# Kernel optimization log

Hardware: AMD Instinct MI355X
Metric: run time of the kernel (lower is better)

The kernel has to match this reference:

```python
import jax, jax.numpy as jnp
import numpy as np
import math

B, WIN, C_IN, C_OUT = 8, 512, 38, 38
D_MODEL, N_HEADS, E_LAYERS, D_FF = 512, 8, 3, 512
EH = D_MODEL // N_HEADS
LN_EPS = 1e-3  # keras LayerNormalization default


def setup_inputs() -> dict:
    key = jax.random.key(0)
    ks = jax.random.split(key, 24)
    s = 0.02
    rn = lambda k, sh: jax.random.normal(k, sh, jnp.float32) * s
    L, d, H = E_LAYERS, D_MODEL, N_HEADS
    return {
        "x": jax.random.normal(ks[0], (B, WIN, C_IN), jnp.float32),
        "conv_k": rn(ks[1], (3, C_IN, d)),
        "Wq": rn(ks[2], (L, d, d)), "bq": jnp.zeros((L, d), jnp.float32),
        "Wk": rn(ks[3], (L, d, d)), "bk": jnp.zeros((L, d), jnp.float32),
        "Wv": rn(ks[4], (L, d, d)), "bv": jnp.zeros((L, d), jnp.float32),
        "Ws": rn(ks[5], (L, d, H)), "bs": jnp.zeros((L, H), jnp.float32),
        "Wo": rn(ks[6], (L, d, d)), "bo": jnp.zeros((L, d), jnp.float32),
        "W1": rn(ks[7], (L, d, D_FF)), "b1": jnp.zeros((L, D_FF), jnp.float32),
        "W2": rn(ks[8], (L, D_FF, d)), "b2": jnp.zeros((L, d), jnp.float32),
        "ln1_g": jnp.ones((L, d), jnp.float32), "ln1_b": jnp.zeros((L, d), jnp.float32),
        "ln2_g": jnp.ones((L, d), jnp.float32), "ln2_b": jnp.zeros((L, d), jnp.float32),
        "lnf_g": jnp.ones((d,), jnp.float32), "lnf_b": jnp.zeros((d,), jnp.float32),
        "Wp": rn(ks[9], (d, C_OUT)), "bp": jnp.zeros((C_OUT,), jnp.float32),
    }


def _layernorm(x, g, b):
    mu = jnp.mean(x, axis=-1, keepdims=True)
    var = jnp.mean((x - mu) ** 2, axis=-1, keepdims=True)
    return (x - mu) * jax.lax.rsqrt(var + LN_EPS) * g + b


def _pos_embedding():
    pos = jnp.arange(WIN, dtype=jnp.float32)[:, None]
    div = jnp.exp(jnp.arange(0, D_MODEL, 2, dtype=jnp.float32) * (-math.log(10000.0) / D_MODEL))
    # interleave sin at even idx, cos at odd idx
    return jnp.stack([jnp.sin(pos * div), jnp.cos(pos * div)], axis=-1).reshape(WIN, D_MODEL)


def reference(x, conv_k, Wq, bq, Wk, bk, Wv, bv, Ws, bs, Wo, bo,
              W1, b1, W2, b2, ln1_g, ln1_b, ln2_g, ln2_b, lnf_g, lnf_b, Wp, bp):
    # --- DataEmbedding: wrap-pad then Conv1D(k=3, valid), plus sinusoidal PE ---
    xp = jnp.concatenate([x[:, -1:], x, x[:, :1]], axis=1)
    h = jax.lax.conv_general_dilated(xp, conv_k, window_strides=(1,), padding='VALID',
                                     dimension_numbers=('NWC', 'WIO', 'NWC'))
    h = h + _pos_embedding()[None]

    idx = jnp.arange(WIN, dtype=jnp.float32)
    dist = jnp.abs(idx[:, None] - idx[None, :])
    scale = 1.0 / math.sqrt(EH)
    inv_sqrt_2pi = 1.0 / math.sqrt(2.0 * math.pi)

    series_l, prior_l, sigma_l = [], [], []
    for i in range(E_LAYERS):
        q = (h @ Wq[i] + bq[i]).reshape(B, WIN, N_HEADS, EH)
        k = (h @ Wk[i] + bk[i]).reshape(B, WIN, N_HEADS, EH)
        v = (h @ Wv[i] + bv[i]).reshape(B, WIN, N_HEADS, EH)
        sig = h @ Ws[i] + bs[i]

        scores = jnp.einsum('blhe,bshe->bhls', q, k)  # mask_flag=False in model
        series = jax.nn.softmax(scores * scale, axis=-1)  # [B, H, L, S]

        sg = jnp.transpose(sig, (0, 2, 1))               # [B, H, L]
        sg = jax.nn.sigmoid(sg * 5.0) + 1e-5
        sg = jnp.power(3.0, sg) - 1.0
        sg4 = jnp.broadcast_to(sg[..., None], (B, N_HEADS, WIN, WIN))
        prior = inv_sqrt_2pi / sg4 * jnp.exp(-(dist ** 2) / (2.0 * sg4 ** 2))

        attn_out = jnp.einsum('bhls,bshd->blhd', series, v).reshape(B, WIN, D_MODEL)
        h = _layernorm(h + attn_out @ Wo[i] + bo[i], ln1_g[i], ln1_b[i])
        y = jax.nn.gelu(h @ W1[i] + b1[i], approximate=False)
        y = y @ W2[i] + b2[i]
        h = _layernorm(h + y, ln2_g[i], ln2_b[i])

        series_l.append(series); prior_l.append(prior); sigma_l.append(sg4)

    h = _layernorm(h, lnf_g, lnf_b)
    out = h @ Wp + bp
    return (out, jnp.stack(series_l), jnp.stack(prior_l), jnp.stack(sigma_l))
```

## Files before the change

### kernel.cpp

```cpp
#include <hip/hip_runtime.h>
#include <math.h>


typedef unsigned short ushort;
typedef __attribute__((ext_vector_type(8))) ushort ushort8;
typedef __attribute__((ext_vector_type(8))) short short8;
typedef __attribute__((ext_vector_type(4))) float float4v;

__device__ inline ushort f2bf(float f) {
  union { float f; unsigned u; } v; v.f = f;
  return (ushort)((v.u + 0x7fffu + ((v.u >> 16) & 1u)) >> 16);
}

__global__ __launch_bounds__(512) void embed_kernel(const float* __restrict__ x,
                                                    const float* __restrict__ ck,
                                                    float* __restrict__ h) {
  int bt = blockIdx.x;
  int b = bt >> 9, t = bt & 511;
  int co = threadIdx.x;
  __shared__ float xs[3][38];
  if (co < 114) {
    int w = co / 38, ci = co - w * 38;
    int r = (t - 1 + w + 512) & 511;
    xs[w][ci] = x[((long)(b << 9) + r) * 38 + ci];
  }
  __syncthreads();
  float acc = 0.f;
#pragma unroll
  for (int w = 0; w < 3; ++w)
#pragma unroll
    for (int ci = 0; ci < 38; ++ci)
      acc = fmaf(xs[w][ci], ck[(w * 38 + ci) * 512 + co], acc);
  float div = expf((float)(co & ~1) * (-9.210340371976184f / 512.f));
  float ang = (float)t * div;
  float pe = (co & 1) ? cosf(ang) : sinf(ang);
  h[(long)bt * 512 + co] = acc + pe;
}

__global__ __launch_bounds__(256) void wcvt_kernel(const float* __restrict__ W,
                                                   ushort* __restrict__ Wt,
                                                   long lstride) {
  int l = blockIdx.z;
  int n = blockIdx.x * 256 + threadIdx.x;
  int k0 = blockIdx.y * 8;
  const float* w = W + (long)l * 262144;
  ushort* o = Wt + (long)l * lstride;
  ushort8 v;
#pragma unroll
  for (int i = 0; i < 8; ++i) v[i] = f2bf(w[(long)(k0 + i) * 512 + n]);
  *(ushort8*)&o[(long)n * 512 + k0] = v;
}

__global__ __launch_bounds__(512) void bcat_kernel(const float* __restrict__ bq,
                                                   const float* __restrict__ bk,
                                                   const float* __restrict__ bv,
                                                   float* __restrict__ bqkv) {
  int l = blockIdx.x, t = threadIdx.x;
  bqkv[l * 1536 + t] = bq[l * 512 + t];
  bqkv[l * 1536 + 512 + t] = bk[l * 512 + t];
  bqkv[l * 1536 + 1024 + t] = bv[l * 512 + t];
}

template <bool ABF16, bool GELU_, bool CBF16>
__global__ __launch_bounds__(256) void gemm_mfma(
    const void* __restrict__ Av, int lda,
    const ushort* __restrict__ B, int ldb,
    const float* __restrict__ bias,
    void* __restrict__ Cv, int ldc,
    int K, float alpha) {
  __shared__ ushort As[64 * 40];
  __shared__ ushort Bs[64 * 40];
  int t = threadIdx.x;
  int m0 = blockIdx.y * 64, n0 = blockIdx.x * 64;
  int w = t >> 6, lane = t & 63;
  int wr = (w >> 1) * 32, wc = (w & 1) * 32;
  int fm = lane & 15, koff = (lane >> 4) * 8;

  float4v acc[2][2] = {{{0.f, 0.f, 0.f, 0.f}, {0.f, 0.f, 0.f, 0.f}},
                       {{0.f, 0.f, 0.f, 0.f}, {0.f, 0.f, 0.f, 0.f}}};
  int sm = t >> 2, skq = (t & 3) * 8;

  for (int k0 = 0; k0 < K; k0 += 32) {
    if (ABF16) {
      const ushort* Ab = (const ushort*)Av;
      *(ushort8*)&As[sm * 40 + skq] =
          *(const ushort8*)&Ab[(long)(m0 + sm) * lda + k0 + skq];
    } else {
      const float* Af = (const float*)Av;
      const float* ap = &Af[(long)(m0 + sm) * lda + k0 + skq];
      float4 x0 = *(const float4*)ap;
      float4 x1 = *(const float4*)(ap + 4);
      ushort8 v;
      v[0] = f2bf(x0.x); v[1] = f2bf(x0.y); v[2] = f2bf(x0.z); v[3] = f2bf(x0.w);
      v[4] = f2bf(x1.x); v[5] = f2bf(x1.y); v[6] = f2bf(x1.z); v[7] = f2bf(x1.w);
      *(ushort8*)&As[sm * 40 + skq] = v;
    }
    *(ushort8*)&Bs[sm * 40 + skq] =
        *(const ushort8*)&B[(long)(n0 + sm) * ldb + k0 + skq];
    __syncthreads();

    short8 a0 = *(const short8*)&As[(wr + fm) * 40 + koff];
    short8 a1 = *(const short8*)&As[(wr + 16 + fm) * 40 + koff];
    short8 b0 = *(const short8*)&Bs[(wc + fm) * 40 + koff];
    short8 b1 = *(const short8*)&Bs[(wc + 16 + fm) * 40 + koff];
    acc[0][0] = __builtin_amdgcn_mfma_f32_16x16x32_bf16(a0, b0, acc[0][0], 0, 0, 0);
    acc[0][1] = __builtin_amdgcn_mfma_f32_16x16x32_bf16(a0, b1, acc[0][1], 0, 0, 0);
    acc[1][0] = __builtin_amdgcn_mfma_f32_16x16x32_bf16(a1, b0, acc[1][0], 0, 0, 0);
    acc[1][1] = __builtin_amdgcn_mfma_f32_16x16x32_bf16(a1, b1, acc[1][1], 0, 0, 0);
    __syncthreads();
  }

#pragma unroll
  for (int j = 0; j < 2; ++j) {
    int col = n0 + wc + 16 * j + fm;
    float bv = bias ? bias[col] : 0.f;
#pragma unroll
    for (int i = 0; i < 2; ++i) {
#pragma unroll
      for (int r = 0; r < 4; ++r) {
        int row = m0 + wr + 16 * i + (lane >> 4) * 4 + r;
        float v = acc[i][j][r] * alpha + bv;
        if (GELU_) v = 0.5f * v * (1.f + erff(v * 0.7071067811865476f));
        if (CBF16)
          ((ushort*)Cv)[(long)row * ldc + col] = f2bf(v);
        else
          ((float*)Cv)[(long)row * ldc + col] = v;
      }
    }
  }
}

__global__ __launch_bounds__(256, 1) void attn_fused(
    const ushort* __restrict__ qkv, const float* __restrict__ sg,
    float* __restrict__ series, float* __restrict__ prior,
    float* __restrict__ sigma, float* __restrict__ t1) {
  __shared__ ushort KPs[36864];
  __shared__ ushort Qs[4608];
  __shared__ ushort Vc[4608];
  __shared__ float red[256];

  int t = threadIdx.x;
  int m0 = blockIdx.x * 64;
  int bh = blockIdx.y;
  int b = bh >> 3, hh = bh & 7;
  int w = t >> 6, lane = t & 63;
  int fm = lane & 15, q4 = lane >> 4;
  int wc = w * 128;
  long rowg = (long)b * 512;

  {
    int row = t >> 2, kq = (t & 3) * 16;
    const ushort* src = &qkv[(rowg + m0 + row) * 1536 + hh * 64 + kq];
    *(ushort8*)&Qs[row * 72 + kq] = *(const ushort8*)src;
    *(ushort8*)&Qs[row * 72 + kq + 8] = *(const ushort8*)(src + 8);
#pragma unroll
    for (int p = 0; p < 8; ++p) {
      int srow = p * 64 + row;
      const ushort* ks = &qkv[(rowg + srow) * 1536 + 512 + hh * 64 + kq];
      *(ushort8*)&KPs[srow * 72 + kq] = *(const ushort8*)ks;
      *(ushort8*)&KPs[srow * 72 + kq + 8] = *(const ushort8*)(ks + 8);
    }
  }
  __syncthreads();

  float4v acc[4][8];
#pragma unroll
  for (int i = 0; i < 4; ++i)
#pragma unroll
    for (int j = 0; j < 8; ++j) acc[i][j] = (float4v){0.f, 0.f, 0.f, 0.f};

#pragma unroll
  for (int ks = 0; ks < 2; ++ks) {
    int ko = ks * 32 + q4 * 8;
    short8 a[4], bfr[8];
#pragma unroll
    for (int i = 0; i < 4; ++i)
      a[i] = *(const short8*)&Qs[(16 * i + fm) * 72 + ko];
#pragma unroll
    for (int j = 0; j < 8; ++j)
      bfr[j] = *(const short8*)&KPs[(wc + 16 * j + fm) * 72 + ko];
#pragma unroll
    for (int i = 0; i < 4; ++i)
#pragma unroll
      for (int j = 0; j < 8; ++j)
        acc[i][j] = __builtin_amdgcn_mfma_f32_16x16x32_bf16(a[i], bfr[j], acc[i][j], 0, 0, 0);
  }

#pragma unroll
  for (int i = 0; i < 4; ++i)
#pragma unroll
    for (int j = 0; j < 8; ++j)
#pragma unroll
      for (int r = 0; r < 4; ++r) acc[i][j][r] *= 0.125f;

  float mrow[4][4];
#pragma unroll
  for (int i = 0; i < 4; ++i)
#pragma unroll
    for (int r = 0; r < 4; ++r) {
      float m = acc[i][0][r];
#pragma unroll
      for (int j = 1; j < 8; ++j) m = fmaxf(m, acc[i][j][r]);
#pragma unroll
      for (int off = 1; off < 16; off <<= 1) m = fmaxf(m, __shfl_xor(m, off));
      mrow[i][r] = m;
    }
  if (fm == 0) {
#pragma unroll
    for (int i = 0; i < 4; ++i)
#pragma unroll
      for (int r = 0; r < 4; ++r)
        red[(16 * i + q4 * 4 + r) * 4 + w] = mrow[i][r];
  }
  __syncthreads();
#pragma unroll
  for (int i = 0; i < 4; ++i)
#pragma unroll
    for (int r = 0; r < 4; ++r) {
      const float* rp = &red[(16 * i + q4 * 4 + r) * 4];
      mrow[i][r] = fmaxf(fmaxf(rp[0], rp[1]), fmaxf(rp[2], rp[3]));
    }
  float lrow[4][4];
#pragma unroll
  for (int i = 0; i < 4; ++i)
#pragma unroll
    for (int r = 0; r < 4; ++r) {
      float s = 0.f;
#pragma unroll
      for (int j = 0; j < 8; ++j) {
        float e = __expf(acc[i][j][r] - mrow[i][r]);
        acc[i][j][r] = e;
        s += e;
      }
#pragma unroll
      for (int off = 1; off < 16; off <<= 1) s += __shfl_xor(s, off);
      lrow[i][r] = s;
    }
  __syncthreads();
  if (fm == 0) {
#pragma unroll
    for (int i = 0; i < 4; ++i)
#pragma unroll
      for (int r = 0; r < 4; ++r)
        red[(16 * i + q4 * 4 + r) * 4 + w] = lrow[i][r];
  }
  __syncthreads();
#pragma unroll
  for (int i = 0; i < 4; ++i)
#pragma unroll
    for (int r = 0; r < 4; ++r) {
      const float* rp = &red[(16 * i + q4 * 4 + r) * 4];
      lrow[i][r] = 1.f / (rp[0] + rp[1] + rp[2] + rp[3]);
    }

  float* serp = series + ((long)bh << 18);
#pragma unroll
  for (int i = 0; i < 4; ++i)
#pragma unroll
    for (int r = 0; r < 4; ++r) {
      int row = 16 * i + q4 * 4 + r;
      float inv = lrow[i][r];
#pragma unroll
      for (int j = 0; j < 8; ++j) {
        int col = wc + 16 * j + fm;
        float v = acc[i][j][r] * inv;
        serp[(long)(m0 + row) * 512 + col] = v;
        KPs[row * 520 + col] = f2bf(v);
      }
    }

  float4v acc2[4] = {{0.f, 0.f, 0.f, 0.f}, {0.f, 0.f, 0.f, 0.f},
                     {0.f, 0.f, 0.f, 0.f}, {0.f, 0.f, 0.f, 0.f}};
  int wn = w * 16;
  int s_local = t >> 2, cgrp = (t & 3) * 16;
  for (int c = 0; c < 8; ++c) {
    __syncthreads();
    const ushort* vs = &qkv[(rowg + c * 64 + s_local) * 1536 + 1024 + hh * 64 + cgrp];
    ushort8 v0 = *(const ushort8*)vs;
    ushort8 v1 = *(const ushort8*)(vs + 8);
#pragma unroll
    for (int e = 0; e < 8; ++e) {
      Vc[(cgrp + e) * 72 + s_local] = v0[e];
      Vc[(cgrp + 8 + e) * 72 + s_local] = v1[e];
    }
    __syncthreads();
#pragma unroll
    for (int ks = 0; ks < 2; ++ks) {
      int ko = ks * 32 + q4 * 8;
      short8 b2 = *(const short8*)&Vc[(wn + fm) * 72 + ko];
#pragma unroll
      for (int i = 0; i < 4; ++i) {
        short8 a2 = *(const short8*)&KPs[(16 * i + fm) * 520 + c * 64 + ko];
        acc2[i] = __builtin_amdgcn_mfma_f32_16x16x32_bf16(a2, b2, acc2[i], 0, 0, 0);
      }
    }
  }
#pragma unroll
  for (int i = 0; i < 4; ++i)
#pragma unroll
    for (int r = 0; r < 4; ++r)
      t1[(rowg + m0 + 16 * i + q4 * 4 + r) * 512 + hh * 64 + wn + fm] = acc2[i][r];

  __syncthreads();
  if (t < 64) {
    float xv = sg[(rowg + m0 + t) * 8 + hh];
    float s = 1.f / (1.f + __expf(-5.f * xv)) + 1e-5f;
    float sgv = expm1f(s * 1.0986122886681098f);
    red[t * 3] = sgv;
    red[t * 3 + 1] = 0.3989422804014327f / sgv;
    red[t * 3 + 2] = 1.f / sgv;
  }
  __syncthreads();
  float* prip = prior + ((long)bh << 18);
  float* sigp = sigma + ((long)bh << 18);
  for (int it = t; it < 8192; it += 256) {
    int row = it >> 7;
    int c4 = (it & 127) << 2;
    float sgv = red[row * 3], inv = red[row * 3 + 1], rinv = red[row * 3 + 2];
    float ig = (float)(m0 + row);
    float4 pv, sv;
#pragma unroll
    for (int e = 0; e < 4; ++e) {
      float dd = ig - (float)(c4 + e);
      float rr = dd * rinv;
      ((float*)&pv)[e] = inv * __expf(-0.5f * rr * rr);
      ((float*)&sv)[e] = sgv;
    }
    *(float4*)&prip[(long)(m0 + row) * 512 + c4] = pv;
    *(float4*)&sigp[(long)(m0 + row) * 512 + c4] = sv;
  }
}

__global__ __launch_bounds__(256) void ln_kernel(const float* __restrict__ x,
                                                 const float* __restrict__ delta,
                                                 const float* __restrict__ g,
                                                 const float* __restrict__ bb,
                                                 float* __restrict__ out) {
  long row = blockIdx.x;
  int tid = threadIdx.x;
  int c = tid * 2;
  float2 xv = *(const float2*)&x[row * 512 + c];
  if (delta) {
    float2 dv = *(const float2*)&delta[row * 512 + c];
    xv.x += dv.x; xv.y += dv.y;
  }
  float s = xv.x + xv.y;
  float q = xv.x * xv.x + xv.y * xv.y;
#pragma unroll
  for (int off = 1; off < 64; off <<= 1) {
    s += __shfl_xor(s, off);
    q += __shfl_xor(q, off);
  }
  __shared__ float red[8];
  int wid = tid >> 6;
  if ((tid & 63) == 0) { red[wid] = s; red[wid + 4] = q; }
  __syncthreads();
  float S = red[0] + red[1] + red[2] + red[3];
  float Q = red[4] + red[5] + red[6] + red[7];
  float mean = S * (1.f / 512.f);
  float var = Q * (1.f / 512.f) - mean * mean;
  float rstd = rsqrtf(var + 1e-3f);
  float2 o;
  o.x = (xv.x - mean) * rstd * g[c] + bb[c];
  o.y = (xv.y - mean) * rstd * g[c + 1] + bb[c + 1];
  *(float2*)&out[row * 512 + c] = o;
}

template <int NOUT>
__global__ __launch_bounds__(256) void gemm_smallN(const float* __restrict__ A,
                                                   const float* __restrict__ W,
                                                   const float* __restrict__ bias,
                                                   float* __restrict__ C) {
  long row = (long)blockIdx.x * 4 + (threadIdx.x >> 6);
  int lane = threadIdx.x & 63;
  float acc[NOUT];
#pragma unroll
  for (int j = 0; j < NOUT; ++j) acc[j] = 0.f;
  for (int k = lane; k < 512; k += 64) {
    float a = A[row * 512 + k];
    const float* wr = W + (long)k * NOUT;
#pragma unroll
    for (int j = 0; j < NOUT; ++j) acc[j] = fmaf(a, wr[j], acc[j]);
  }
#pragma unroll
  for (int j = 0; j < NOUT; ++j)
#pragma unroll
    for (int off = 32; off; off >>= 1) acc[j] += __shfl_xor(acc[j], off);
  if (lane == 0) {
#pragma unroll
    for (int j = 0; j < NOUT; ++j) C[row * NOUT + j] = acc[j] + bias[j];
  }
}

extern "C" void kernel_launch(void* const* d_in, const int* in_sizes, int n_in,
                              void* d_out, int out_size, void* d_ws, size_t ws_size,
                              hipStream_t stream) {
  (void)in_sizes; (void)n_in; (void)out_size; (void)ws_size;
  const float* x    = (const float*)d_in[0];
  const float* ck   = (const float*)d_in[1];
  const float* Wq   = (const float*)d_in[2];
  const float* bq   = (const float*)d_in[3];
  const float* Wk   = (const float*)d_in[4];
  const float* bk   = (const float*)d_in[5];
  const float* Wv   = (const float*)d_in[6];
  const float* bv   = (const float*)d_in[7];
  const float* Wsw  = (const float*)d_in[8];
  const float* bsw  = (const float*)d_in[9];
  const float* Wo   = (const float*)d_in[10];
  const float* bo   = (const float*)d_in[11];
  const float* W1   = (const float*)d_in[12];
  const float* b1   = (const float*)d_in[13];
  const float* W2   = (const float*)d_in[14];
  const float* b2   = (const float*)d_in[15];
  const float* ln1g = (const float*)d_in[16];
  const float* ln1b = (const float*)d_in[17];
  const float* ln2g = (const float*)d_in[18];
  const float* ln2b = (const float*)d_in[19];
  const float* lnfg = (const float*)d_in[20];
  const float* lnfb = (const float*)d_in[21];
  const float* Wp   = (const float*)d_in[22];
  const float* bp   = (const float*)d_in[23];
  float* out = (float*)d_out;

  float* h    = (float*)d_ws;
  float* t1   = h + 2097152;
  float* t2   = t1 + 2097152;
  float* sg   = t2 + 2097152;
  float* bqkv = sg + 32768;
  ushort* qkv  = (ushort*)(bqkv + 4608);
  ushort* wqkv = qkv + 6291456;
  ushort* wo3  = wqkv + 2359296;
  ushort* w13  = wo3 + 786432;
  ushort* w23  = w13 + 786432;

  float* series0 = out + 155648;
  float* prior0  = out + 50487296;
  float* sigma0  = out + 100818944;

  dim3 gW(2, 64, 3);
  wcvt_kernel<<<gW, 256, 0, stream>>>(Wq, wqkv, 786432);
  wcvt_kernel<<<gW, 256, 0, stream>>>(Wk, wqkv + 262144, 786432);
  wcvt_kernel<<<gW, 256, 0, stream>>>(Wv, wqkv + 524288, 786432);
  wcvt_kernel<<<gW, 256, 0, stream>>>(Wo, wo3, 262144);
  wcvt_kernel<<<gW, 256, 0, stream>>>(W1, w13, 262144);
  wcvt_kernel<<<gW, 256, 0, stream>>>(W2, w23, 262144);
  bcat_kernel<<<3, 512, 0, stream>>>(bq, bk, bv, bqkv);

  embed_kernel<<<4096, 512, 0, stream>>>(x, ck, h);

  dim3 gQKV(24, 64, 1);
  dim3 gFull(8, 64, 1);
  dim3 gAttn(8, 64, 1);

  for (int l = 0; l < 3; ++l) {
    float* ser = series0 + (long)l * 16777216;
    float* pri = prior0  + (long)l * 16777216;
    float* sgm = sigma0  + (long)l * 16777216;

    gemm_mfma<false, false, true><<<gQKV, 256, 0, stream>>>(
        h, 512, wqkv + (long)l * 786432, 512, bqkv + l * 1536, qkv, 1536, 512, 1.f);
    gemm_smallN<8><<<1024, 256, 0, stream>>>(h, Wsw + (long)l * 4096, bsw + l * 8, sg);
    attn_fused<<<gAttn, 256, 0, stream>>>(qkv, sg, ser, pri, sgm, t1);
    gemm_mfma<false, false, false><<<gFull, 256, 0, stream>>>(
        t1, 512, wo3 + (long)l * 262144, 512, bo + (long)l * 512, t2, 512, 512, 1.f);
    ln_kernel<<<4096, 256, 0, stream>>>(h, t2, ln1g + l * 512, ln1b + l * 512, h);
    gemm_mfma<false, true, false><<<gFull, 256, 0, stream>>>(
        h, 512, w13 + (long)l * 262144, 512, b1 + (long)l * 512, t1, 512, 512, 1.f);
    gemm_mfma<false, false, false><<<gFull, 256, 0, stream>>>(
        t1, 512, w23 + (long)l * 262144, 512, b2 + (long)l * 512, t2, 512, 512, 1.f);
    ln_kernel<<<4096, 256, 0, stream>>>(h, t2, ln2g + l * 512, ln2b + l * 512, h);
  }

  ln_kernel<<<4096, 256, 0, stream>>>(h, nullptr, lnfg, lnfb, t1);
  gemm_smallN<38><<<1024, 256, 0, stream>>>(t1, Wp, bp, out);
}
```

Measured before the change: 1.085 ms.

## Use bf16 activations, async LDS-loading 128x64 GEMM, and pre-transposed V in attention

Producers (embedding, layernorm, attention, FFN1) now also write bf16 copies of their activations. GEMMs are replaced by a 128x64-tile kernel that fills LDS with global_load_lds and skips the in-kernel fp32-to-bf16 conversion. A separate kernel transposes V per head so the attention kernel can read Q, K and V^T straight from global memory instead of staging them in LDS. The attention kernel's shared-memory footprint shrinks and its launch bound allows two blocks per CU, in exchange for an extra launch and bf16 rounding of intermediate activations.

```diff
diff --git a/kernel.cpp b/kernel.cpp
--- a/kernel.cpp
+++ b/kernel.cpp
@@ -12,9 +12,16 @@
   return (ushort)((v.u + 0x7fffu + ((v.u >> 16) & 1u)) >> 16);
 }
 
+__device__ inline void gload16(const void* g, void* l) {
+  __builtin_amdgcn_global_load_lds(
+      (const __attribute__((address_space(1))) unsigned int*)g,
+      (__attribute__((address_space(3))) unsigned int*)l, 16, 0, 0);
+}
+
 __global__ __launch_bounds__(512) void embed_kernel(const float* __restrict__ x,
                                                     const float* __restrict__ ck,
-                                                    float* __restrict__ h) {
+                                                    float* __restrict__ h,
+                                                    ushort* __restrict__ hb) {
   int bt = blockIdx.x;
   int b = bt >> 9, t = bt & 511;
   int co = threadIdx.x;
@@ -34,7 +41,9 @@
   float div = expf((float)(co & ~1) * (-9.210340371976184f / 512.f));
   float ang = (float)t * div;
   float pe = (co & 1) ? cosf(ang) : sinf(ang);
-  h[(long)bt * 512 + co] = acc + pe;
+  float o = acc + pe;
+  h[(long)bt * 512 + co] = o;
+  hb[(long)bt * 512 + co] = f2bf(o);
 }
 
 __global__ __launch_bounds__(256) void wcvt_kernel(const float* __restrict__ W,
@@ -61,52 +70,51 @@
   bqkv[l * 1536 + 1024 + t] = bv[l * 512 + t];
 }
 
-template <bool ABF16, bool GELU_, bool CBF16>
-__global__ __launch_bounds__(256) void gemm_mfma(
-    const void* __restrict__ Av, int lda,
+template <bool GELU_, bool CBF16>
+__global__ __launch_bounds__(256) void gemm_bt(
+    const ushort* __restrict__ A, int lda,
     const ushort* __restrict__ B, int ldb,
     const float* __restrict__ bias,
-    void* __restrict__ Cv, int ldc,
-    int K, float alpha) {
-  __shared__ ushort As[64 * 40];
-  __shared__ ushort Bs[64 * 40];
+    void* __restrict__ Cv, int ldc, int K) {
+  __shared__ ushort As[4096];
+  __shared__ ushort Bs[2048];
   int t = threadIdx.x;
-  int m0 = blockIdx.y * 64, n0 = blockIdx.x * 64;
+  int m0 = blockIdx.y * 128, n0 = blockIdx.x * 64;
   int w = t >> 6, lane = t & 63;
-  int wr = (w >> 1) * 32, wc = (w & 1) * 32;
-  int fm = lane & 15, koff = (lane >> 4) * 8;
-
-  float4v acc[2][2] = {{{0.f, 0.f, 0.f, 0.f}, {0.f, 0.f, 0.f, 0.f}},
-                       {{0.f, 0.f, 0.f, 0.f}, {0.f, 0.f, 0.f, 0.f}}};
-  int sm = t >> 2, skq = (t & 3) * 8;
+  int wr = (w >> 1) * 64, wc = (w & 1) * 32;
+  int fm = lane & 15, q4 = lane >> 4;
+  float4v acc[4][2];
+#pragma unroll
+  for (int i = 0; i < 4; ++i)
+#pragma unroll
+    for (int j = 0; j < 2; ++j) acc[i][j] = (float4v){0.f, 0.f, 0.f, 0.f};
+
+  int kk = (lane & 3) * 8;
+  const ushort* ga0 = &A[(long)(m0 + w * 32 + (lane >> 2)) * lda + kk];
+  const ushort* ga1 = ga0 + (long)16 * lda;
+  const ushort* gb = &B[(long)(n0 + w * 16 + (lane >> 2)) * ldb + kk];
+  ushort* lA0 = &As[(w * 2) * 512];
+  ushort* lA1 = &As[(w * 2 + 1) * 512];
+  ushort* lB = &Bs[w * 512];
 
   for (int k0 = 0; k0 < K; k0 += 32) {
-    if (ABF16) {
-      const ushort* Ab = (const ushort*)Av;
-      *(ushort8*)&As[sm * 40 + skq] =
-          *(const ushort8*)&Ab[(long)(m0 + sm) * lda + k0 + skq];
-    } else {
-      const float* Af = (const float*)Av;
-      const float* ap = &Af[(long)(m0 + sm) * lda + k0 + skq];
-      float4 x0 = *(const float4*)ap;
-      float4 x1 = *(const float4*)(ap + 4);
-      ushort8 v;
-      v[0] = f2bf(x0.x); v[1] = f2bf(x0.y); v[2] = f2bf(x0.z); v[3] = f2bf(x0.w);
-      v[4] = f2bf(x1.x); v[5] = f2bf(x1.y); v[6] = f2bf(x1.z); v[7] = f2bf(x1.w);
-      *(ushort8*)&As[sm * 40 + skq] = v;
-    }
-    *(ushort8*)&Bs[sm * 40 + skq] =
-        *(const ushort8*)&B[(long)(n0 + sm) * ldb + k0 + skq];
+    gload16(ga0, lA0);
+    gload16(ga1, lA1);
+    gload16(gb, lB);
+    ga0 += 32; ga1 += 32; gb += 32;
     __syncthreads();
-
-    short8 a0 = *(const short8*)&As[(wr + fm) * 40 + koff];
-    short8 a1 = *(const short8*)&As[(wr + 16 + fm) * 40 + koff];
-    short8 b0 = *(const short8*)&Bs[(wc + fm) * 40 + koff];
-    short8 b1 = *(const short8*)&Bs[(wc + 16 + fm) * 40 + koff];
-    acc[0][0] = __builtin_amdgcn_mfma_f32_16x16x32_bf16(a0, b0, acc[0][0], 0, 0, 0);
-    acc[0][1] = __builtin_amdgcn_mfma_f32_16x16x32_bf16(a0, b1, acc[0][1], 0, 0, 0);
-    acc[1][0] = __builtin_amdgcn_mfma_f32_16x16x32_bf16(a1, b0, acc[1][0], 0, 0, 0);
-    acc[1][1] = __builtin_amdgcn_mfma_f32_16x16x32_bf16(a1, b1, acc[1][1], 0, 0, 0);
+    short8 a[4], bfr[2];
+#pragma unroll
+    for (int i = 0; i < 4; ++i)
+      a[i] = *(const short8*)&As[(wr + 16 * i + fm) * 32 + q4 * 8];
+#pragma unroll
+    for (int j = 0; j < 2; ++j)
+      bfr[j] = *(const short8*)&Bs[(wc + 16 * j + fm) * 32 + q4 * 8];
+#pragma unroll
+    for (int i = 0; i < 4; ++i)
+#pragma unroll
+      for (int j = 0; j < 2; ++j)
+        acc[i][j] = __builtin_amdgcn_mfma_f32_16x16x32_bf16(a[i], bfr[j], acc[i][j], 0, 0, 0);
     __syncthreads();
   }
 
@@ -115,11 +123,11 @@
     int col = n0 + wc + 16 * j + fm;
     float bv = bias ? bias[col] : 0.f;
 #pragma unroll
-    for (int i = 0; i < 2; ++i) {
+    for (int i = 0; i < 4; ++i) {
 #pragma unroll
       for (int r = 0; r < 4; ++r) {
-        int row = m0 + wr + 16 * i + (lane >> 4) * 4 + r;
-        float v = acc[i][j][r] * alpha + bv;
+        int row = m0 + wr + 16 * i + q4 * 4 + r;
+        float v = acc[i][j][r] + bv;
         if (GELU_) v = 0.5f * v * (1.f + erff(v * 0.7071067811865476f));
         if (CBF16)
           ((ushort*)Cv)[(long)row * ldc + col] = f2bf(v);
@@ -130,13 +138,35 @@
   }
 }
 
-__global__ __launch_bounds__(256, 1) void attn_fused(
-    const ushort* __restrict__ qkv, const float* __restrict__ sg,
+__global__ __launch_bounds__(256) void vtrans_kernel(const ushort* __restrict__ qkv,
+                                                     ushort* __restrict__ vT) {
+  int c = blockIdx.x, bh = blockIdx.y;
+  int b = bh >> 3, hh = bh & 7;
+  __shared__ ushort tile[64][72];
+  int t = threadIdx.x;
+  int sr = t >> 2, d0 = (t & 3) * 16;
+  const ushort* src = &qkv[((long)b * 512 + c * 64 + sr) * 1536 + 1024 + hh * 64 + d0];
+  *(ushort8*)&tile[sr][d0] = *(const ushort8*)src;
+  *(ushort8*)&tile[sr][d0 + 8] = *(const ushort8*)(src + 8);
+  __syncthreads();
+  int d = t >> 2, s0 = (t & 3) * 16;
+  ushort8 v0, v1;
+#pragma unroll
+  for (int e = 0; e < 8; ++e) {
+    v0[e] = tile[s0 + e][d];
+    v1[e] = tile[s0 + 8 + e][d];
+  }
+  ushort* dst = &vT[((long)bh * 64 + d) * 512 + c * 64 + s0];
+  *(ushort8*)dst = v0;
+  *(ushort8*)(dst + 8) = v1;
+}
+
+__global__ __launch_bounds__(256, 2) void attn_fused(
+    const ushort* __restrict__ qkv, const ushort* __restrict__ vT,
+    const float* __restrict__ sg,
     float* __restrict__ series, float* __restrict__ prior,
-    float* __restrict__ sigma, float* __restrict__ t1) {
-  __shared__ ushort KPs[36864];
-  __shared__ ushort Qs[4608];
-  __shared__ ushort Vc[4608];
+    float* __restrict__ sigma, ushort* __restrict__ t1b) {
+  __shared__ ushort Ps[64 * 520];
   __shared__ float red[256];
 
   int t = threadIdx.x;
@@ -148,37 +178,24 @@
   int wc = w * 128;
   long rowg = (long)b * 512;
 
-  {
-    int row = t >> 2, kq = (t & 3) * 16;
-    const ushort* src = &qkv[(rowg + m0 + row) * 1536 + hh * 64 + kq];
-    *(ushort8*)&Qs[row * 72 + kq] = *(const ushort8*)src;
-    *(ushort8*)&Qs[row * 72 + kq + 8] = *(const ushort8*)(src + 8);
-#pragma unroll
-    for (int p = 0; p < 8; ++p) {
-      int srow = p * 64 + row;
-      const ushort* ks = &qkv[(rowg + srow) * 1536 + 512 + hh * 64 + kq];
-      *(ushort8*)&KPs[srow * 72 + kq] = *(const ushort8*)ks;
-      *(ushort8*)&KPs[srow * 72 + kq + 8] = *(const ushort8*)(ks + 8);
-    }
-  }
-  __syncthreads();
-
   float4v acc[4][8];
 #pragma unroll
   for (int i = 0; i < 4; ++i)
 #pragma unroll
     for (int j = 0; j < 8; ++j) acc[i][j] = (float4v){0.f, 0.f, 0.f, 0.f};
 
+  const ushort* qbase = &qkv[(rowg + m0) * 1536 + hh * 64];
+  const ushort* kbase = &qkv[rowg * 1536 + 512 + hh * 64];
 #pragma unroll
   for (int ks = 0; ks < 2; ++ks) {
     int ko = ks * 32 + q4 * 8;
     short8 a[4], bfr[8];
 #pragma unroll
     for (int i = 0; i < 4; ++i)
-      a[i] = *(const short8*)&Qs[(16 * i + fm) * 72 + ko];
+      a[i] = *(const short8*)&qbase[(long)(16 * i + fm) * 1536 + ko];
 #pragma unroll
     for (int j = 0; j < 8; ++j)
-      bfr[j] = *(const short8*)&KPs[(wc + 16 * j + fm) * 72 + ko];
+      bfr[j] = *(const short8*)&kbase[(long)(wc + 16 * j + fm) * 1536 + ko];
 #pragma unroll
     for (int i = 0; i < 4; ++i)
 #pragma unroll
@@ -265,32 +282,24 @@
         int col = wc + 16 * j + fm;
         float v = acc[i][j][r] * inv;
         serp[(long)(m0 + row) * 512 + col] = v;
-        KPs[row * 520 + col] = f2bf(v);
+        Ps[row * 520 + col] = f2bf(v);
       }
     }
+  __syncthreads();
 
   float4v acc2[4] = {{0.f, 0.f, 0.f, 0.f}, {0.f, 0.f, 0.f, 0.f},
                      {0.f, 0.f, 0.f, 0.f}, {0.f, 0.f, 0.f, 0.f}};
   int wn = w * 16;
-  int s_local = t >> 2, cgrp = (t & 3) * 16;
+  const ushort* vbase = &vT[((long)bh * 64 + wn + fm) * 512];
+#pragma unroll
   for (int c = 0; c < 8; ++c) {
-    __syncthreads();
-    const ushort* vs = &qkv[(rowg + c * 64 + s_local) * 1536 + 1024 + hh * 64 + cgrp];
-    ushort8 v0 = *(const ushort8*)vs;
-    ushort8 v1 = *(const ushort8*)(vs + 8);
-#pragma unroll
-    for (int e = 0; e < 8; ++e) {
-      Vc[(cgrp + e) * 72 + s_local] = v0[e];
-      Vc[(cgrp + 8 + e) * 72 + s_local] = v1[e];
-    }
-    __syncthreads();
 #pragma unroll
     for (int ks = 0; ks < 2; ++ks) {
       int ko = ks * 32 + q4 * 8;
-      short8 b2 = *(const short8*)&Vc[(wn + fm) * 72 + ko];
+      short8 b2 = *(const short8*)&vbase[c * 64 + ko];
 #pragma unroll
       for (int i = 0; i < 4; ++i) {
-        short8 a2 = *(const short8*)&KPs[(16 * i + fm) * 520 + c * 64 + ko];
+        short8 a2 = *(const short8*)&Ps[(16 * i + fm) * 520 + c * 64 + ko];
         acc2[i] = __builtin_amdgcn_mfma_f32_16x16x32_bf16(a2, b2, acc2[i], 0, 0, 0);
       }
     }
@@ -299,9 +308,9 @@
   for (int i = 0; i < 4; ++i)
 #pragma unroll
     for (int r = 0; r < 4; ++r)
-      t1[(rowg + m0 + 16 * i + q4 * 4 + r) * 512 + hh * 64 + wn + fm] = acc2[i][r];
-
-  __syncthreads();
+      t1b[(rowg + m0 + 16 * i + q4 * 4 + r) * 512 + hh * 64 + wn + fm] =
+          f2bf(acc2[i][r]);
+
   if (t < 64) {
     float xv = sg[(rowg + m0 + t) * 8 + hh];
     float s = 1.f / (1.f + __expf(-5.f * xv)) + 1e-5f;
@@ -335,7 +344,8 @@
                                                  const float* __restrict__ delta,
                                                  const float* __restrict__ g,
                                                  const float* __restrict__ bb,
-                                                 float* __restrict__ out) {
+                                                 float* __restrict__ out,
+                                                 ushort* __restrict__ hb) {
   long row = blockIdx.x;
   int tid = threadIdx.x;
   int c = tid * 2;
@@ -364,6 +374,10 @@
   o.x = (xv.x - mean) * rstd * g[c] + bb[c];
   o.y = (xv.y - mean) * rstd * g[c + 1] + bb[c + 1];
   *(float2*)&out[row * 512 + c] = o;
+  if (hb) {
+    unsigned pk = ((unsigned)f2bf(o.y) << 16) | (unsigned)f2bf(o.x);
+    ((unsigned*)hb)[row * 256 + tid] = pk;
+  }
 }
 
 template <int NOUT>
@@ -432,6 +446,9 @@
   ushort* wo3  = wqkv + 2359296;
   ushort* w13  = wo3 + 786432;
   ushort* w23  = w13 + 786432;
+  ushort* t1b = (ushort*)t1;
+  ushort* hb  = (ushort*)(t1 + 1048576);
+  ushort* vT  = (ushort*)t2;
 
   float* series0 = out + 155648;
   float* prior0  = out + 50487296;
@@ -446,10 +463,11 @@
   wcvt_kernel<<<gW, 256, 0, stream>>>(W2, w23, 262144);
   bcat_kernel<<<3, 512, 0, stream>>>(bq, bk, bv, bqkv);
 
-  embed_kernel<<<4096, 512, 0, stream>>>(x, ck, h);
-
-  dim3 gQKV(24, 64, 1);
-  dim3 gFull(8, 64, 1);
+  embed_kernel<<<4096, 512, 0, stream>>>(x, ck, h, hb);
+
+  dim3 gQKV(24, 32, 1);
+  dim3 gFull(8, 32, 1);
+  dim3 gVT(8, 64, 1);
   dim3 gAttn(8, 64, 1);
 
   for (int l = 0; l < 3; ++l) {
@@ -457,20 +475,21 @@
     float* pri = prior0  + (long)l * 16777216;
     float* sgm = sigma0  + (long)l * 16777216;
 
-    gemm_mfma<false, false, true><<<gQKV, 256, 0, stream>>>(
-        h, 512, wqkv + (long)l * 786432, 512, bqkv + l * 1536, qkv, 1536, 512, 1.f);
+    gemm_bt<false, true><<<gQKV, 256, 0, stream>>>(
+        hb, 512, wqkv + (long)l * 786432, 512, bqkv + l * 1536, qkv, 1536, 512);
     gemm_smallN<8><<<1024, 256, 0, stream>>>(h, Wsw + (long)l * 4096, bsw + l * 8, sg);
-    attn_fused<<<gAttn, 256, 0, stream>>>(qkv, sg, ser, pri, sgm, t1);
-    gemm_mfma<false, false, false><<<gFull, 256, 0, stream>>>(
-        t1, 512, wo3 + (long)l * 262144, 512, bo + (long)l * 512, t2, 512, 512, 1.f);
-    ln_kernel<<<4096, 256, 0, stream>>>(h, t2, ln1g + l * 512, ln1b + l * 512, h);
-    gemm_mfma<false, true, false><<<gFull, 256, 0, stream>>>(
-        h, 512, w13 + (long)l * 262144, 512, b1 + (long)l * 512, t1, 512, 512, 1.f);
-    gemm_mfma<false, false, false><<<gFull, 256, 0, stream>>>(
-        t1, 512, w23 + (long)l * 262144, 512, b2 + (long)l * 512, t2, 512, 512, 1.f);
-    ln_kernel<<<4096, 256, 0, stream>>>(h, t2, ln2g + l * 512, ln2b + l * 512, h);
-  }
-
-  ln_kernel<<<4096, 256, 0, stream>>>(h, nullptr, lnfg, lnfb, t1);
+    vtrans_kernel<<<gVT, 256, 0, stream>>>(qkv, vT);
+    attn_fused<<<gAttn, 256, 0, stream>>>(qkv, vT, sg, ser, pri, sgm, t1b);
+    gemm_bt<false, false><<<gFull, 256, 0, stream>>>(
+        t1b, 512, wo3 + (long)l * 262144, 512, bo + (long)l * 512, t2, 512, 512);
+    ln_kernel<<<4096, 256, 0, stream>>>(h, t2, ln1g + l * 512, ln1b + l * 512, h, hb);
+    gemm_bt<true, true><<<gFull, 256, 0, stream>>>(
+        hb, 512, w13 + (long)l * 262144, 512, b1 + (long)l * 512, t1b, 512, 512);
+    gemm_bt<false, false><<<gFull, 256, 0, stream>>>(
+        t1b, 512, w23 + (long)l * 262144, 512, b2 + (long)l * 512, t2, 512, 512);
+    ln_kernel<<<4096, 256, 0, stream>>>(h, t2, ln2g + l * 512, ln2b + l * 512, h, hb);
+  }
+
+  ln_kernel<<<4096, 256, 0, stream>>>(h, nullptr, lnfg, lnfb, t1, nullptr);
   gemm_smallN<38><<<1024, 256, 0, stream>>>(t1, Wp, bp, out);
 }
```

New measurement: 1.045 ms. 3.7% less time.
